# Kernel optimization log

Measured on AMD Instinct MI355X. Metric: run time of the kernel, lower is better.

The kernel has to match this reference:

```python
import jax, jax.numpy as jnp
import numpy as np

NUM_PTS = 8   # num_points_per_face
K = 5         # self.k


def _sq_dist(x, y):
    # squared euclidean distance matrix (Nx, Ny); matches torch.cdist**2 / sum((a-b)**2)
    x2 = jnp.sum(x * x, axis=1)[:, None]
    y2 = jnp.sum(y * y, axis=1)[None, :]
    d = x2 + y2 - 2.0 * (x @ y.T)
    return jnp.maximum(d, 0.0)


def setup_inputs() -> dict:
    key = jax.random.key(0)
    k1, k2, k3, k4, k5, k6, k7 = jax.random.split(key, 7)
    V, Fs, Ft = 2048, 4096, 4096
    return {
        "source_vertices": jax.random.normal(k1, (1, V, 3), dtype=jnp.float32),
        "source_faces": jax.random.randint(k2, (Fs, 3), 0, V),
        "target_vertices": jax.random.normal(k3, (1, V, 3), dtype=jnp.float32),
        "target_faces": jax.random.randint(k4, (3, Ft), 0, V),
        "face_probs": jax.random.uniform(k5, (Fs,), dtype=jnp.float32),
        "r1u": jax.random.uniform(k6, (Fs, NUM_PTS), dtype=jnp.float32),
        "r2u": jax.random.uniform(k7, (Fs, NUM_PTS), dtype=jnp.float32),
    }


def reference(source_vertices, source_faces, target_vertices, target_faces, face_probs, r1u, r2u):
    sv = source_vertices[0]                 # (V, 3)
    tv = target_vertices[0]                 # (V, 3)
    tf = target_faces.T                     # (Ft, 3)
    Fs = source_faces.shape[0]

    src_bc = sv[source_faces].mean(axis=1)  # (Fs, 3) source barycenters
    tgt_bc = tv[tf].mean(axis=1)            # (Ft, 3) target barycenters

    # ---- forward loss: prob-weighted min squared distance to target barycenters
    d_fwd = _sq_dist(src_bc, tgt_bc)        # (Fs, Ft)
    forward_loss = jnp.sum(face_probs * jnp.min(d_fwd, axis=1))

    # ---- sample points from triangles via barycentric coords
    r1 = jnp.sqrt(r1u)
    w1 = 1.0 - r1
    w2 = r1 * (1.0 - r2u)
    w3 = r1 * r2u
    v1 = sv[source_faces[:, 0]]             # (Fs, 3)
    v2 = sv[source_faces[:, 1]]
    v3 = sv[source_faces[:, 2]]
    pts = (w1[..., None] * v1[:, None] + w2[..., None] * v2[:, None]
           + w3[..., None] * v3[:, None]).reshape(-1, 3)   # (P, 3), P = Fs*NUM_PTS
    pt_faces = jnp.repeat(jnp.arange(Fs), NUM_PTS)          # (P,)
    pt_probs = face_probs[pt_faces]                         # (P,)

    # ---- reverse loss, batched over all P points
    d_src = _sq_dist(pts, src_bc)                           # (P, Fs)
    neg_d, idx = jax.lax.top_k(-d_src, K + 1)               # K+1 smallest distances
    tri_dists = -neg_d                                      # (P, K+1)
    mask = idx != pt_faces[:, None]                         # exclude own face
    has_self = jnp.any(~mask, axis=1)
    excl_pos = jnp.where(has_self, jnp.argmin(mask, axis=1), K + 1)  # (P,)
    t = jnp.arange(K)
    sel = t[None, :] + (t[None, :] >= excl_pos[:, None]).astype(jnp.int32)  # (P, K)
    valid_dists = jnp.take_along_axis(tri_dists, sel, axis=1)   # (P, K)
    valid_idx = jnp.take_along_axis(idx, sel, axis=1)           # (P, K)
    valid_probs = face_probs[valid_idx]                         # (P, K)

    min_tgt = jnp.min(_sq_dist(pts, tgt_bc), axis=1)            # (P,)

    reverse_loss = jnp.sum(pt_probs * min_tgt
                           + (1.0 - pt_probs) * jnp.mean(valid_probs * valid_dists, axis=1))
    return forward_loss + reverse_loss
```

## Files before the change

### kernel.cpp

```cpp
#include <hip/hip_runtime.h>
#include <math.h>

#define FS 4096
#define FT 4096
#define TS 1024
#define BIGF 3.0e38f
#define KEYINF 0xFFFFFFFFu

__device__ __forceinline__ unsigned umin32(unsigned a, unsigned b) { return a < b ? a : b; }
__device__ __forceinline__ unsigned umax32(unsigned a, unsigned b) { return a < b ? b : a; }

__device__ __forceinline__ unsigned med3u(unsigned a, unsigned b, unsigned c) {
    unsigned d;
    asm("v_med3_u32 %0, %1, %2, %3" : "=v"(d) : "v"(a), "v"(b), "v"(c));
    return d;
}

__device__ __forceinline__ float block_reduce_sum(float v) {
    __shared__ float s[8];
    for (int o = 32; o > 0; o >>= 1) v += __shfl_down(v, o, 64);
    int lane = threadIdx.x & 63, wid = threadIdx.x >> 6;
    if (lane == 0) s[wid] = v;
    __syncthreads();
    int nw = blockDim.x >> 6;
    v = (threadIdx.x < (unsigned)nw) ? s[threadIdx.x] : 0.f;
    if (wid == 0)
        for (int o = 4; o > 0; o >>= 1) v += __shfl_down(v, o, 64);
    return v;
}

#define CE(x, y) { unsigned _n = umin32(x, y); y = umax32(x, y); x = _n; }

__device__ __forceinline__ void merge16(unsigned s[6]) {
    #pragma unroll
    for (int m = 1; m <= 8; m <<= 1) {
        unsigned b0 = __shfl_xor(s[0], m, 64), b1 = __shfl_xor(s[1], m, 64);
        unsigned b2 = __shfl_xor(s[2], m, 64), b3 = __shfl_xor(s[3], m, 64);
        unsigned b4 = __shfl_xor(s[4], m, 64), b5 = __shfl_xor(s[5], m, 64);
        unsigned l0 = s[0], l1 = s[1];
        unsigned l2 = umin32(s[2], b5), l3 = umin32(s[3], b4);
        unsigned l4 = umin32(s[4], b3), l5 = umin32(s[5], b2);
        unsigned l6 = b1, l7 = b0;
        CE(l0, l4) CE(l1, l5) CE(l2, l6) CE(l3, l7)
        CE(l0, l2) CE(l1, l3) CE(l4, l6) CE(l5, l7)
        CE(l0, l1) CE(l2, l3) CE(l4, l5) CE(l6, l7)
        s[0] = l0; s[1] = l1; s[2] = l2; s[3] = l3; s[4] = l4; s[5] = l5;
    }
}

__global__ __launch_bounds__(256) void k_prep(
        const float* __restrict__ sv, const int* __restrict__ sf,
        const float* __restrict__ tv, const int* __restrict__ tf,
        float4* __restrict__ sbc2, float4* __restrict__ tbc2,
        float4* __restrict__ sbcr, float* __restrict__ out) {
    int i = blockIdx.x * blockDim.x + threadIdx.x;
    if (i == 0) out[0] = 0.f;
    if (i >= FS) return;
    const float third = 1.f / 3.f;
    int a = sf[3*i], b = sf[3*i+1], c = sf[3*i+2];
    float x = (sv[3*a  ] + sv[3*b  ] + sv[3*c  ]) * third;
    float y = (sv[3*a+1] + sv[3*b+1] + sv[3*c+1]) * third;
    float z = (sv[3*a+2] + sv[3*b+2] + sv[3*c+2]) * third;
    float n2 = x*x + y*y + z*z;
    sbc2[i] = make_float4(-2.f*x, -2.f*y, -2.f*z, n2);
    sbcr[i] = make_float4(x, y, z, n2);
    int ta = tf[i], tb = tf[FT + i], tc = tf[2*FT + i];
    float tx = (tv[3*ta  ] + tv[3*tb  ] + tv[3*tc  ]) * third;
    float ty = (tv[3*ta+1] + tv[3*tb+1] + tv[3*tc+1]) * third;
    float tz = (tv[3*ta+2] + tv[3*tb+2] + tv[3*tc+2]) * third;
    tbc2[i] = make_float4(-2.f*tx, -2.f*ty, -2.f*tz, tx*tx + ty*ty + tz*tz);
}

__global__ __launch_bounds__(256, 2) void k_main(
        const float* __restrict__ sv, const int* __restrict__ sf,
        const float* __restrict__ fp,
        const float* __restrict__ r1u, const float* __restrict__ r2u,
        const float4* __restrict__ sbc2, const float4* __restrict__ tbc2,
        const float4* __restrict__ sbcr, float* __restrict__ out) {
    __shared__ float4 tile[TS];
    __shared__ float fmins[16];
    int tid  = threadIdx.x;
    int seg  = tid & 15;
    int slot = tid >> 4;
    int blk  = blockIdx.x;

    int face = blk*8 + (slot >> 1);
    int a = sf[3*face], b = sf[3*face+1], c = sf[3*face+2];
    float ax = sv[3*a], ay = sv[3*a+1], az = sv[3*a+2];
    float bx = sv[3*b], by = sv[3*b+1], bz = sv[3*b+2];
    float cx = sv[3*c], cy = sv[3*c+1], cz = sv[3*c+2];
    float4 r14 = ((const float4*)r1u)[blk*16 + slot];
    float4 r24 = ((const float4*)r2u)[blk*16 + slot];
    float px[4], py[4], pz[4], p2[4];
    {
        float r1a[4] = {r14.x, r14.y, r14.z, r14.w};
        float r2a[4] = {r24.x, r24.y, r24.z, r24.w};
        #pragma unroll
        for (int i = 0; i < 4; ++i) {
            float r1 = sqrtf(r1a[i]);
            float w1 = 1.f - r1, w2 = r1 * (1.f - r2a[i]), w3 = r1 * r2a[i];
            px[i] = w1*ax + w2*bx + w3*cx;
            py[i] = w1*ay + w2*by + w3*cy;
            pz[i] = w1*az + w2*bz + w3*cz;
            p2[i] = px[i]*px[i] + py[i]*py[i] + pz[i]*pz[i];
        }
    }
    int fface = blk*8 + (slot & 7);
    float4 fbc = sbcr[fface];

    unsigned srt[4][6];
    #pragma unroll
    for (int i = 0; i < 4; ++i)
        #pragma unroll
        for (int k = 0; k < 6; ++k) srt[i][k] = KEYINF;

    float4 pre[4];
    #pragma unroll
    for (int j = 0; j < 4; ++j) pre[j] = sbc2[tid + j*256];

    for (int t0 = 0; t0 < FS; t0 += TS) {
        #pragma unroll
        for (int j = 0; j < 4; ++j) tile[tid + j*256] = pre[j];
        __syncthreads();
        if (t0 + TS < FS) {
            #pragma unroll
            for (int j = 0; j < 4; ++j) pre[j] = sbc2[t0 + TS + tid + j*256];
        } else {
            #pragma unroll
            for (int j = 0; j < 4; ++j) pre[j] = tbc2[tid + j*256];
        }
        unsigned jj = (unsigned)(t0 + seg);
        #pragma unroll 4
        for (int jp = 0; jp < TS/16; ++jp) {
            float4 c4 = tile[(jp << 4) + seg];
            #pragma unroll
            for (int i = 0; i < 4; ++i) {
                float v = fmaf(px[i], c4.x, fmaf(py[i], c4.y, fmaf(pz[i], c4.z, c4.w)));
                float d = fmaxf(v + p2[i], 0.f);
                unsigned k = (__float_as_uint(d) & 0xFFFFF000u) | jj;
                unsigned n0 = umin32(srt[i][0], k);
                unsigned n1 = med3u(srt[i][0], srt[i][1], k);
                unsigned n2 = med3u(srt[i][1], srt[i][2], k);
                unsigned n3 = med3u(srt[i][2], srt[i][3], k);
                unsigned n4 = med3u(srt[i][3], srt[i][4], k);
                unsigned n5 = med3u(srt[i][4], srt[i][5], k);
                srt[i][0]=n0; srt[i][1]=n1; srt[i][2]=n2;
                srt[i][3]=n3; srt[i][4]=n4; srt[i][5]=n5;
            }
            jj += 16;
        }
        __syncthreads();
    }

    float vtr[4] = {BIGF, BIGF, BIGF, BIGF};
    float vf = BIGF;
    for (int t0 = 0; t0 < FT; t0 += TS) {
        #pragma unroll
        for (int j = 0; j < 4; ++j) tile[tid + j*256] = pre[j];
        __syncthreads();
        if (t0 + TS < FT) {
            #pragma unroll
            for (int j = 0; j < 4; ++j) pre[j] = tbc2[t0 + TS + tid + j*256];
        }
        #pragma unroll 4
        for (int jp = 0; jp < TS/16; ++jp) {
            float4 c4 = tile[(jp << 4) + seg];
            #pragma unroll
            for (int i = 0; i < 4; ++i) {
                float v = fmaf(px[i], c4.x, fmaf(py[i], c4.y, fmaf(pz[i], c4.z, c4.w)));
                vtr[i] = fminf(vtr[i], v);
            }
            float v5 = fmaf(fbc.x, c4.x, fmaf(fbc.y, c4.y, fmaf(fbc.z, c4.z, c4.w)));
            vf = fminf(vf, v5);
        }
        __syncthreads();
    }

    #pragma unroll
    for (int i = 0; i < 4; ++i) {
        float v = vtr[i];
        v = fminf(v, __shfl_xor(v, 1, 64));
        v = fminf(v, __shfl_xor(v, 2, 64));
        v = fminf(v, __shfl_xor(v, 4, 64));
        v = fminf(v, __shfl_xor(v, 8, 64));
        vtr[i] = v;
        merge16(srt[i]);
    }
    vf = fminf(vf, __shfl_xor(vf, 1, 64));
    vf = fminf(vf, __shfl_xor(vf, 2, 64));
    vf = fminf(vf, __shfl_xor(vf, 4, 64));
    vf = fminf(vf, __shfl_xor(vf, 8, 64));
    if (seg == 0) fmins[slot] = vf;
    __syncthreads();

    float contrib = 0.f;
    if (seg == 0) {
        float pf = fp[face];
        #pragma unroll
        for (int i = 0; i < 4; ++i) {
            int   q0 = srt[i][0] & 0xFFF, q1 = srt[i][1] & 0xFFF, q2 = srt[i][2] & 0xFFF;
            int   q3 = srt[i][3] & 0xFFF, q4 = srt[i][4] & 0xFFF, q5 = srt[i][5] & 0xFFF;
            float d0 = __uint_as_float(srt[i][0] & 0xFFFFF000u);
            float d1 = __uint_as_float(srt[i][1] & 0xFFFFF000u);
            float d2 = __uint_as_float(srt[i][2] & 0xFFFFF000u);
            float d3 = __uint_as_float(srt[i][3] & 0xFFFFF000u);
            float d4 = __uint_as_float(srt[i][4] & 0xFFFFF000u);
            float d5 = __uint_as_float(srt[i][5] & 0xFFFFF000u);

            int skip = 5;
            if      (q0 == face) skip = 0;
            else if (q1 == face) skip = 1;
            else if (q2 == face) skip = 2;
            else if (q3 == face) skip = 3;
            else if (q4 == face) skip = 4;

            float s = 0.f;
            if (skip != 0) s += fp[q0] * d0;
            if (skip != 1) s += fp[q1] * d1;
            if (skip != 2) s += fp[q2] * d2;
            if (skip != 3) s += fp[q3] * d3;
            if (skip != 4) s += fp[q4] * d4;
            if (skip != 5) s += fp[q5] * d5;

            float mtd = fmaxf(vtr[i] + p2[i], 0.f);
            contrib += pf * mtd + (1.f - pf) * (s * 0.2f);
        }
    }
    if (tid < 8) {
        float m = fminf(fmins[tid], fmins[tid + 8]);
        int ff = blk*8 + tid;
        contrib += fp[ff] * fmaxf(m + sbcr[ff].w, 0.f);
    }

    float tot = block_reduce_sum(contrib);
    if (tid == 0) atomicAdd(out, tot);
}

extern "C" void kernel_launch(void* const* d_in, const int* in_sizes, int n_in,
                              void* d_out, int out_size, void* d_ws, size_t ws_size,
                              hipStream_t stream) {
    const float* sv  = (const float*)d_in[0];
    const int*   sf  = (const int*)  d_in[1];
    const float* tv  = (const float*)d_in[2];
    const int*   tf  = (const int*)  d_in[3];
    const float* fp  = (const float*)d_in[4];
    const float* r1u = (const float*)d_in[5];
    const float* r2u = (const float*)d_in[6];
    float* out = (float*)d_out;

    char* ws = (char*)d_ws;
    float4* sbc2 = (float4*)(ws);
    float4* tbc2 = (float4*)(ws + 65536);
    float4* sbcr = (float4*)(ws + 131072);

    k_prep<<<16,  256, 0, stream>>>(sv, sf, tv, tf, sbc2, tbc2, sbcr, out);
    k_main<<<512, 256, 0, stream>>>(sv, sf, fp, r1u, r2u, sbc2, tbc2, sbcr, out);
}
```

Before: 136.9 us.

## Split work into more blocks with fewer points per thread and separate forward-loss blocks

Each thread now handles 2 sample points instead of 4, so the grid grows from 512 to 1024 point blocks, and 128 extra blocks compute the forward-loss minima separately. The register prefetch of the next tile is dropped and launch bounds are raised to 6 blocks per SM. The aim is more waves in flight and better use of the many CUs. In exchange, each block loads the shared tile twice as often per point, and loads are no longer overlapped with compute.

```diff
diff --git a/kernel.cpp b/kernel.cpp
--- a/kernel.cpp
+++ b/kernel.cpp
@@ -71,165 +71,160 @@
     tbc2[i] = make_float4(-2.f*tx, -2.f*ty, -2.f*tz, tx*tx + ty*ty + tz*tz);
 }
 
-__global__ __launch_bounds__(256, 2) void k_main(
+__global__ __launch_bounds__(256, 6) void k_main(
         const float* __restrict__ sv, const int* __restrict__ sf,
         const float* __restrict__ fp,
         const float* __restrict__ r1u, const float* __restrict__ r2u,
         const float4* __restrict__ sbc2, const float4* __restrict__ tbc2,
         const float4* __restrict__ sbcr, float* __restrict__ out) {
     __shared__ float4 tile[TS];
-    __shared__ float fmins[16];
     int tid  = threadIdx.x;
     int seg  = tid & 15;
     int slot = tid >> 4;
-    int blk  = blockIdx.x;
-
-    int face = blk*8 + (slot >> 1);
-    int a = sf[3*face], b = sf[3*face+1], c = sf[3*face+2];
-    float ax = sv[3*a], ay = sv[3*a+1], az = sv[3*a+2];
-    float bx = sv[3*b], by = sv[3*b+1], bz = sv[3*b+2];
-    float cx = sv[3*c], cy = sv[3*c+1], cz = sv[3*c+2];
-    float4 r14 = ((const float4*)r1u)[blk*16 + slot];
-    float4 r24 = ((const float4*)r2u)[blk*16 + slot];
-    float px[4], py[4], pz[4], p2[4];
-    {
-        float r1a[4] = {r14.x, r14.y, r14.z, r14.w};
-        float r2a[4] = {r24.x, r24.y, r24.z, r24.w};
+    float contrib = 0.f;
+
+    if (blockIdx.x < 1024) {
+        int pt0  = blockIdx.x * 32 + slot * 2;
+        int face = pt0 >> 3;
+
+        int a = sf[3*face], b = sf[3*face+1], c = sf[3*face+2];
+        float ax = sv[3*a], ay = sv[3*a+1], az = sv[3*a+2];
+        float bx = sv[3*b], by = sv[3*b+1], bz = sv[3*b+2];
+        float cx = sv[3*c], cy = sv[3*c+1], cz = sv[3*c+2];
+        float2 r1p = ((const float2*)r1u)[pt0 >> 1];
+        float2 r2p = ((const float2*)r2u)[pt0 >> 1];
+        float px[2], py[2], pz[2], p2[2];
+        {
+            float r1a[2] = {r1p.x, r1p.y};
+            float r2a[2] = {r2p.x, r2p.y};
+            #pragma unroll
+            for (int i = 0; i < 2; ++i) {
+                float r1 = sqrtf(r1a[i]);
+                float w1 = 1.f - r1, w2 = r1 * (1.f - r2a[i]), w3 = r1 * r2a[i];
+                px[i] = w1*ax + w2*bx + w3*cx;
+                py[i] = w1*ay + w2*by + w3*cy;
+                pz[i] = w1*az + w2*bz + w3*cz;
+                p2[i] = px[i]*px[i] + py[i]*py[i] + pz[i]*pz[i];
+            }
+        }
+
+        unsigned srt[2][6];
         #pragma unroll
-        for (int i = 0; i < 4; ++i) {
-            float r1 = sqrtf(r1a[i]);
-            float w1 = 1.f - r1, w2 = r1 * (1.f - r2a[i]), w3 = r1 * r2a[i];
-            px[i] = w1*ax + w2*bx + w3*cx;
-            py[i] = w1*ay + w2*by + w3*cy;
-            pz[i] = w1*az + w2*bz + w3*cz;
-            p2[i] = px[i]*px[i] + py[i]*py[i] + pz[i]*pz[i];
-        }
-    }
-    int fface = blk*8 + (slot & 7);
-    float4 fbc = sbcr[fface];
-
-    unsigned srt[4][6];
-    #pragma unroll
-    for (int i = 0; i < 4; ++i)
+        for (int i = 0; i < 2; ++i)
+            #pragma unroll
+            for (int k = 0; k < 6; ++k) srt[i][k] = KEYINF;
+
+        for (int t0 = 0; t0 < FS; t0 += TS) {
+            #pragma unroll
+            for (int j = 0; j < 4; ++j) tile[tid + j*256] = sbc2[t0 + tid + j*256];
+            __syncthreads();
+            unsigned jj = (unsigned)(t0 + seg);
+            #pragma unroll 4
+            for (int jp = 0; jp < TS/16; ++jp) {
+                float4 c4 = tile[(jp << 4) + seg];
+                #pragma unroll
+                for (int i = 0; i < 2; ++i) {
+                    float v = fmaf(px[i], c4.x, fmaf(py[i], c4.y, fmaf(pz[i], c4.z, c4.w)));
+                    float d = fmaxf(v + p2[i], 0.f);
+                    unsigned k = (__float_as_uint(d) & 0xFFFFF000u) | jj;
+                    unsigned n0 = umin32(srt[i][0], k);
+                    unsigned n1 = med3u(srt[i][0], srt[i][1], k);
+                    unsigned n2 = med3u(srt[i][1], srt[i][2], k);
+                    unsigned n3 = med3u(srt[i][2], srt[i][3], k);
+                    unsigned n4 = med3u(srt[i][3], srt[i][4], k);
+                    unsigned n5 = med3u(srt[i][4], srt[i][5], k);
+                    srt[i][0]=n0; srt[i][1]=n1; srt[i][2]=n2;
+                    srt[i][3]=n3; srt[i][4]=n4; srt[i][5]=n5;
+                }
+                jj += 16;
+            }
+            __syncthreads();
+        }
+
+        float vtr[2] = {BIGF, BIGF};
+        for (int t0 = 0; t0 < FT; t0 += TS) {
+            #pragma unroll
+            for (int j = 0; j < 4; ++j) tile[tid + j*256] = tbc2[t0 + tid + j*256];
+            __syncthreads();
+            #pragma unroll 4
+            for (int jp = 0; jp < TS/16; ++jp) {
+                float4 c4 = tile[(jp << 4) + seg];
+                #pragma unroll
+                for (int i = 0; i < 2; ++i) {
+                    float v = fmaf(px[i], c4.x, fmaf(py[i], c4.y, fmaf(pz[i], c4.z, c4.w)));
+                    vtr[i] = fminf(vtr[i], v);
+                }
+            }
+            __syncthreads();
+        }
+
         #pragma unroll
-        for (int k = 0; k < 6; ++k) srt[i][k] = KEYINF;
-
-    float4 pre[4];
-    #pragma unroll
-    for (int j = 0; j < 4; ++j) pre[j] = sbc2[tid + j*256];
-
-    for (int t0 = 0; t0 < FS; t0 += TS) {
+        for (int i = 0; i < 2; ++i) {
+            float v = vtr[i];
+            v = fminf(v, __shfl_xor(v, 1, 64));
+            v = fminf(v, __shfl_xor(v, 2, 64));
+            v = fminf(v, __shfl_xor(v, 4, 64));
+            v = fminf(v, __shfl_xor(v, 8, 64));
+            vtr[i] = v;
+            merge16(srt[i]);
+        }
+
+        if (seg == 0) {
+            float pf = fp[face];
+            #pragma unroll
+            for (int i = 0; i < 2; ++i) {
+                int   q0 = srt[i][0] & 0xFFF, q1 = srt[i][1] & 0xFFF, q2 = srt[i][2] & 0xFFF;
+                int   q3 = srt[i][3] & 0xFFF, q4 = srt[i][4] & 0xFFF, q5 = srt[i][5] & 0xFFF;
+                float d0 = __uint_as_float(srt[i][0] & 0xFFFFF000u);
+                float d1 = __uint_as_float(srt[i][1] & 0xFFFFF000u);
+                float d2 = __uint_as_float(srt[i][2] & 0xFFFFF000u);
+                float d3 = __uint_as_float(srt[i][3] & 0xFFFFF000u);
+                float d4 = __uint_as_float(srt[i][4] & 0xFFFFF000u);
+                float d5 = __uint_as_float(srt[i][5] & 0xFFFFF000u);
+
+                int skip = 5;
+                if      (q0 == face) skip = 0;
+                else if (q1 == face) skip = 1;
+                else if (q2 == face) skip = 2;
+                else if (q3 == face) skip = 3;
+                else if (q4 == face) skip = 4;
+
+                float s = 0.f;
+                if (skip != 0) s += fp[q0] * d0;
+                if (skip != 1) s += fp[q1] * d1;
+                if (skip != 2) s += fp[q2] * d2;
+                if (skip != 3) s += fp[q3] * d3;
+                if (skip != 4) s += fp[q4] * d4;
+                if (skip != 5) s += fp[q5] * d5;
+
+                float mtd = fmaxf(vtr[i] + p2[i], 0.f);
+                contrib += pf * mtd + (1.f - pf) * (s * 0.2f);
+            }
+        }
+    } else {
+        int f0 = (blockIdx.x - 1024) * 32 + slot * 2;
+        float4 bc0 = sbcr[f0], bc1 = sbcr[f0 + 1];
+        float v0 = BIGF, v1 = BIGF;
+        for (int t0 = 0; t0 < FT; t0 += TS) {
+            #pragma unroll
+            for (int j = 0; j < 4; ++j) tile[tid + j*256] = tbc2[t0 + tid + j*256];
+            __syncthreads();
+            #pragma unroll 4
+            for (int jp = 0; jp < TS/16; ++jp) {
+                float4 c4 = tile[(jp << 4) + seg];
+                v0 = fminf(v0, fmaf(bc0.x, c4.x, fmaf(bc0.y, c4.y, fmaf(bc0.z, c4.z, c4.w))));
+                v1 = fminf(v1, fmaf(bc1.x, c4.x, fmaf(bc1.y, c4.y, fmaf(bc1.z, c4.z, c4.w))));
+            }
+            __syncthreads();
+        }
         #pragma unroll
-        for (int j = 0; j < 4; ++j) tile[tid + j*256] = pre[j];
-        __syncthreads();
-        if (t0 + TS < FS) {
-            #pragma unroll
-            for (int j = 0; j < 4; ++j) pre[j] = sbc2[t0 + TS + tid + j*256];
-        } else {
-            #pragma unroll
-            for (int j = 0; j < 4; ++j) pre[j] = tbc2[tid + j*256];
-        }
-        unsigned jj = (unsigned)(t0 + seg);
-        #pragma unroll 4
-        for (int jp = 0; jp < TS/16; ++jp) {
-            float4 c4 = tile[(jp << 4) + seg];
-            #pragma unroll
-            for (int i = 0; i < 4; ++i) {
-                float v = fmaf(px[i], c4.x, fmaf(py[i], c4.y, fmaf(pz[i], c4.z, c4.w)));
-                float d = fmaxf(v + p2[i], 0.f);
-                unsigned k = (__float_as_uint(d) & 0xFFFFF000u) | jj;
-                unsigned n0 = umin32(srt[i][0], k);
-                unsigned n1 = med3u(srt[i][0], srt[i][1], k);
-                unsigned n2 = med3u(srt[i][1], srt[i][2], k);
-                unsigned n3 = med3u(srt[i][2], srt[i][3], k);
-                unsigned n4 = med3u(srt[i][3], srt[i][4], k);
-                unsigned n5 = med3u(srt[i][4], srt[i][5], k);
-                srt[i][0]=n0; srt[i][1]=n1; srt[i][2]=n2;
-                srt[i][3]=n3; srt[i][4]=n4; srt[i][5]=n5;
-            }
-            jj += 16;
-        }
-        __syncthreads();
-    }
-
-    float vtr[4] = {BIGF, BIGF, BIGF, BIGF};
-    float vf = BIGF;
-    for (int t0 = 0; t0 < FT; t0 += TS) {
-        #pragma unroll
-        for (int j = 0; j < 4; ++j) tile[tid + j*256] = pre[j];
-        __syncthreads();
-        if (t0 + TS < FT) {
-            #pragma unroll
-            for (int j = 0; j < 4; ++j) pre[j] = tbc2[t0 + TS + tid + j*256];
-        }
-        #pragma unroll 4
-        for (int jp = 0; jp < TS/16; ++jp) {
-            float4 c4 = tile[(jp << 4) + seg];
-            #pragma unroll
-            for (int i = 0; i < 4; ++i) {
-                float v = fmaf(px[i], c4.x, fmaf(py[i], c4.y, fmaf(pz[i], c4.z, c4.w)));
-                vtr[i] = fminf(vtr[i], v);
-            }
-            float v5 = fmaf(fbc.x, c4.x, fmaf(fbc.y, c4.y, fmaf(fbc.z, c4.z, c4.w)));
-            vf = fminf(vf, v5);
-        }
-        __syncthreads();
-    }
-
-    #pragma unroll
-    for (int i = 0; i < 4; ++i) {
-        float v = vtr[i];
-        v = fminf(v, __shfl_xor(v, 1, 64));
-        v = fminf(v, __shfl_xor(v, 2, 64));
-        v = fminf(v, __shfl_xor(v, 4, 64));
-        v = fminf(v, __shfl_xor(v, 8, 64));
-        vtr[i] = v;
-        merge16(srt[i]);
-    }
-    vf = fminf(vf, __shfl_xor(vf, 1, 64));
-    vf = fminf(vf, __shfl_xor(vf, 2, 64));
-    vf = fminf(vf, __shfl_xor(vf, 4, 64));
-    vf = fminf(vf, __shfl_xor(vf, 8, 64));
-    if (seg == 0) fmins[slot] = vf;
-    __syncthreads();
-
-    float contrib = 0.f;
-    if (seg == 0) {
-        float pf = fp[face];
-        #pragma unroll
-        for (int i = 0; i < 4; ++i) {
-            int   q0 = srt[i][0] & 0xFFF, q1 = srt[i][1] & 0xFFF, q2 = srt[i][2] & 0xFFF;
-            int   q3 = srt[i][3] & 0xFFF, q4 = srt[i][4] & 0xFFF, q5 = srt[i][5] & 0xFFF;
-            float d0 = __uint_as_float(srt[i][0] & 0xFFFFF000u);
-            float d1 = __uint_as_float(srt[i][1] & 0xFFFFF000u);
-            float d2 = __uint_as_float(srt[i][2] & 0xFFFFF000u);
-            float d3 = __uint_as_float(srt[i][3] & 0xFFFFF000u);
-            float d4 = __uint_as_float(srt[i][4] & 0xFFFFF000u);
-            float d5 = __uint_as_float(srt[i][5] & 0xFFFFF000u);
-
-            int skip = 5;
-            if      (q0 == face) skip = 0;
-            else if (q1 == face) skip = 1;
-            else if (q2 == face) skip = 2;
-            else if (q3 == face) skip = 3;
-            else if (q4 == face) skip = 4;
-
-            float s = 0.f;
-            if (skip != 0) s += fp[q0] * d0;
-            if (skip != 1) s += fp[q1] * d1;
-            if (skip != 2) s += fp[q2] * d2;
-            if (skip != 3) s += fp[q3] * d3;
-            if (skip != 4) s += fp[q4] * d4;
-            if (skip != 5) s += fp[q5] * d5;
-
-            float mtd = fmaxf(vtr[i] + p2[i], 0.f);
-            contrib += pf * mtd + (1.f - pf) * (s * 0.2f);
-        }
-    }
-    if (tid < 8) {
-        float m = fminf(fmins[tid], fmins[tid + 8]);
-        int ff = blk*8 + tid;
-        contrib += fp[ff] * fmaxf(m + sbcr[ff].w, 0.f);
+        for (int m = 1; m <= 8; m <<= 1) {
+            v0 = fminf(v0, __shfl_xor(v0, m, 64));
+            v1 = fminf(v1, __shfl_xor(v1, m, 64));
+        }
+        if (seg == 0)
+            contrib = fp[f0]     * fmaxf(v0 + bc0.w, 0.f)
+                    + fp[f0 + 1] * fmaxf(v1 + bc1.w, 0.f);
     }
 
     float tot = block_reduce_sum(contrib);
@@ -253,6 +248,6 @@
     float4* tbc2 = (float4*)(ws + 65536);
     float4* sbcr = (float4*)(ws + 131072);
 
-    k_prep<<<16,  256, 0, stream>>>(sv, sf, tv, tf, sbc2, tbc2, sbcr, out);
-    k_main<<<512, 256, 0, stream>>>(sv, sf, fp, r1u, r2u, sbc2, tbc2, sbcr, out);
-}
+    k_prep<<<16,   256, 0, stream>>>(sv, sf, tv, tf, sbc2, tbc2, sbcr, out);
+    k_main<<<1152, 256, 0, stream>>>(sv, sf, fp, r1u, r2u, sbc2, tbc2, sbcr, out);
+}
```

New measurement: 125.1 us. 8.6% less time.
